# Kernel tuning notes

Measured on AMD Instinct MI355X. Metric: run time of the kernel, lower is better.

## Reference

```python
import jax, jax.numpy as jnp
import numpy as np

EPS = 1e-5

def _bin_act(x):
    # sign() forward, clipped straight-through estimator backward
    xc = jnp.clip(x, -1.0, 1.0)
    return xc + jax.lax.stop_gradient(jnp.sign(x) - xc)

def _bin_w(w):
    # XNOR-style: sign(w) scaled by per-output-channel mean(|w|); identity STE
    alpha = jnp.mean(jnp.abs(w), axis=(1, 2, 3), keepdims=True)
    return w + jax.lax.stop_gradient(jnp.sign(w) * alpha - w)

def _conv(x, w, stride, padding, groups):
    return jax.lax.conv_general_dilated(
        x, w, window_strides=(stride, stride),
        padding=[(padding, padding), (padding, padding)],
        feature_group_count=groups,
        dimension_numbers=('NCHW', 'OIHW', 'NCHW'))

def _binconv(x, w, stride, padding, groups):
    return _conv(_bin_act(x), _bin_w(w), stride, padding, groups)

def _bn(x, g, b, m, v):
    # eval-mode BatchNorm2d
    inv = g / jnp.sqrt(v + EPS)
    return x * inv[None, :, None, None] + (b - m * inv)[None, :, None, None]


def setup_inputs() -> dict:
    key = jax.random.key(0)
    ks = jax.random.split(key, 20)
    inp, oup = 256, 512
    d = {}
    d['x'] = jax.random.normal(ks[0], (64, inp, 28, 28), jnp.float32)
    d['w1'] = jax.random.normal(ks[1], (inp, 16, 3, 3), jnp.float32) * 0.1  # grouped, groups=inp/16
    d['w2'] = jax.random.normal(ks[2], (oup, inp, 1, 1), jnp.float32) * 0.05
    d['w3'] = jax.random.normal(ks[3], (oup, oup, 1, 1), jnp.float32) * 0.05
    for i, (name, c) in enumerate([('1', inp), ('2', oup), ('3', oup)]):
        d['g' + name] = jax.random.uniform(ks[4 + 4 * i], (c,), jnp.float32, 0.5, 1.5)
        d['b' + name] = jax.random.normal(ks[5 + 4 * i], (c,), jnp.float32) * 0.1
        d['m' + name] = jax.random.normal(ks[6 + 4 * i], (c,), jnp.float32) * 0.1
        d['v' + name] = jax.random.uniform(ks[7 + 4 * i], (c,), jnp.float32, 0.5, 1.5)
    return d


def reference(x, w1, w2, w3, g1, b1, m1, v1, g2, b2, m2, v2, g3, b3, m3, v3):
    inp = x.shape[1]
    groups = inp // 16
    # conv1 (binary grouped 3x3) + bn1 + residual + hardtanh
    out = _bn(_binconv(x, w1, 1, 1, groups), g1, b1, m1, v1)
    out = jnp.clip(out + x, -1.0, 1.0)
    # conv2 (binary 1x1, inp->oup) + bn2 + hardtanh
    out = jnp.clip(_bn(_binconv(out, w2, 1, 0, 1), g2, b2, m2, v2), -1.0, 1.0)
    res = out
    # conv3 (binary 1x1, oup->oup) + bn3 + residual + hardtanh
    out = _bn(_binconv(out, w3, 1, 0, 1), g3, b3, m3, v3)
    return jnp.clip(out + res, -1.0, 1.0)
```

## Files before the change

### kernel.cpp

```cpp
#include <hip/hip_runtime.h>
#include <stdint.h>

#define C1 256
#define C2 512
#define P_ 784
#define TAU 1e-6
#define PT 32
#define NT 25


__global__ __launch_bounds__(256) void prep(
    const float* __restrict__ w1, const float* __restrict__ w2, const float* __restrict__ w3,
    const float* __restrict__ g1, const float* __restrict__ b1, const float* __restrict__ m1, const float* __restrict__ v1,
    const float* __restrict__ g2, const float* __restrict__ b2, const float* __restrict__ m2, const float* __restrict__ v2,
    const float* __restrict__ g3, const float* __restrict__ b3, const float* __restrict__ m3, const float* __restrict__ v3,
    double* __restrict__ sc1d, double* __restrict__ bi1d,
    int* __restrict__ T2, float* __restrict__ sc2f, float* __restrict__ bi2f,
    float* __restrict__ sc3f, float* __restrict__ bi3f,
    uint16_t* __restrict__ wb1, uint32_t* __restrict__ bw2, uint32_t* __restrict__ bw3,
    unsigned long long* __restrict__ amin)
{
    int bid = blockIdx.x, t = threadIdx.x;
    if (bid == 0 && t == 0) amin[0] = ~0ULL;
    if (bid == 0) {
        int co = t;
        const float* wp = w1 + (size_t)co * 144;
        double s = 0.0;
        for (int k = 0; k < 144; k++) s += fabs((double)wp[k]);
        double alpha = s / 144.0;
        double iv = (double)g1[co] / sqrt((double)v1[co] + 1e-5);
        sc1d[co] = alpha * iv;
        bi1d[co] = (double)b1[co] - (double)m1[co] * iv;
        for (int tap = 0; tap < 9; tap++) {
            uint32_t wv = 0;
            for (int ci = 0; ci < 16; ci++) wv |= (uint32_t)(wp[ci * 9 + tap] < 0.f) << ci;
            wb1[co * 9 + tap] = (uint16_t)wv;
        }
    } else if (bid <= 2) {
        int co = (bid - 1) * 256 + t;
        const float* wp = w2 + (size_t)co * 256;
        double s = 0.0;
        for (int k = 0; k < 256; k++) s += fabs((double)wp[k]);
        double alpha = s / 256.0;
        double iv = (double)g2[co] / sqrt((double)v2[co] + 1e-5);
        double sc = alpha * iv;
        double bi = (double)b2[co] - (double)m2[co] * iv;
        int T = -257;
        while (T <= 257 && fma((double)T, sc, bi) < 0.0) T++;
        T2[co] = T;
        sc2f[co] = (float)sc;
        bi2f[co] = (float)bi;
        for (int wd = 0; wd < 8; wd++) {
            uint32_t wv = 0;
            for (int j = 0; j < 32; j++) wv |= (uint32_t)(wp[wd * 32 + j] < 0.f) << j;
            bw2[co * 8 + wd] = wv;
        }
    } else {
        int co = (bid - 3) * 256 + t;
        const float* wp = w3 + (size_t)co * 512;
        double s = 0.0;
        for (int k = 0; k < 512; k++) s += fabs((double)wp[k]);
        double alpha = s / 512.0;
        double iv = (double)g3[co] / sqrt((double)v3[co] + 1e-5);
        sc3f[co] = (float)(alpha * iv);
        bi3f[co] = (float)((double)b3[co] - (double)m3[co] * iv);
        for (int wd = 0; wd < 16; wd++) {
            uint32_t wv = 0;
            for (int j = 0; j < 32; j++) wv |= (uint32_t)(wp[wd * 32 + j] < 0.f) << j;
            bw3[co * 16 + wd] = wv;
        }
    }
}

__global__ __launch_bounds__(256) void k1(
    const float* __restrict__ x,
    const double* __restrict__ sc1d, const double* __restrict__ bi1d,
    const uint16_t* __restrict__ wb1,
    uint16_t* __restrict__ pk1, unsigned long long* __restrict__ amin)
{
    __shared__ uint32_t xzb[30][30];
    __shared__ uint16_t wbl[16][9];
    __shared__ double scs[16], bis[16];
    __shared__ float scf[16], bif[16];

    int g = blockIdx.x, n = blockIdx.y, t = threadIdx.x;

    for (int idx = t; idx < 900; idx += 256) ((uint32_t*)xzb)[idx] = 0;
    if (t < 144) ((uint16_t*)wbl)[t] = wb1[g * 144 + t];
    if (t < 16) {
        scs[t] = sc1d[g * 16 + t]; bis[t] = bi1d[g * 16 + t];
        scf[t] = (float)scs[t];    bif[t] = (float)bis[t];
    }
    __syncthreads();

    const float* xg = x + ((size_t)n * C1 + g * 16) * P_;
    float xr[4][16];
    #pragma unroll
    for (int i = 0; i < 4; i++) {
        int p = t + 256 * i;
        if (p < P_) {
            uint32_t sb = 0, nb = 0;
            #pragma unroll
            for (int ci = 0; ci < 16; ci++) {
                float xv = xg[ci * P_ + p];
                xr[i][ci] = xv;
                sb |= (uint32_t)(xv < 0.f) << ci;
                nb |= (uint32_t)(xv != 0.f) << ci;
            }
            int h = p / 28, w = p - 28 * h;
            xzb[h + 1][w + 1] = sb | (nb << 16);
        }
    }
    __syncthreads();

    uint16_t* pko = pk1 + ((size_t)n * 16 + g) * P_;
    #pragma unroll
    for (int i = 0; i < 4; i++) {
        int p = t + 256 * i;
        if (p < P_) {
            int h = p / 28, w = p - 28 * h;
            uint32_t xv9[9], zv9[9];
            int Z = 0;
            #pragma unroll
            for (int kh = 0; kh < 3; kh++)
                #pragma unroll
                for (int kw = 0; kw < 3; kw++) {
                    int k = kh * 3 + kw;
                    uint32_t xz = xzb[h + kh][w + kw];
                    xv9[k] = xz & 0xFFFFu;
                    zv9[k] = xz >> 16;
                    Z += __popc(zv9[k]);
                }
            uint32_t word = 0;
            #pragma unroll
            for (int co = 0; co < 16; co++) {
                int pd = 0;
                #pragma unroll
                for (int k = 0; k < 9; k++)
                    pd += __popc((xv9[k] ^ (uint32_t)wbl[co][k]) & zv9[k]);
                int S = Z - 2 * pd;
                float vf = __fmaf_rn((float)S, scf[co], bif[co]) + xr[i][co];
                uint32_t neg;
                if (fabsf(vf) < 1e-3f) {
                    double v = fma((double)S, scs[co], bis[co]) + (double)xr[i][co];
                    v = fmin(fmax(v, -1.0), 1.0);
                    double m = fabs(v);
                    if (m < TAU) {
                        unsigned long long pk =
                            ((unsigned long long)__float_as_uint((float)m) << 32) |
                            (unsigned long long)((uint32_t)(n * C1 + g * 16 + co) * (uint32_t)P_ + (uint32_t)p);
                        atomicMin(amin, pk);
                    }
                    neg = (v < 0.0);
                } else {
                    neg = (vf < 0.f);
                }
                word |= neg << co;
            }
            pko[p] = (uint16_t)word;
        }
    }
}

#define POP2(xp) (__popc((xp)[0] ^ wa.x) + __popc((xp)[1] ^ wa.y) + __popc((xp)[2] ^ wa.z) + __popc((xp)[3] ^ wa.w) \
                + __popc((xp)[4] ^ wb.x) + __popc((xp)[5] ^ wb.y) + __popc((xp)[6] ^ wb.z) + __popc((xp)[7] ^ wb.w))
#define POP3(yp) (__popc((yp)[0] ^ w3a.x) + __popc((yp)[1] ^ w3a.y) + __popc((yp)[2] ^ w3a.z) + __popc((yp)[3] ^ w3a.w) \
                + __popc((yp)[4] ^ w3b.x) + __popc((yp)[5] ^ w3b.y) + __popc((yp)[6] ^ w3b.z) + __popc((yp)[7] ^ w3b.w) \
                + __popc((yp)[8] ^ w3c.x) + __popc((yp)[9] ^ w3c.y) + __popc((yp)[10] ^ w3c.z) + __popc((yp)[11] ^ w3c.w) \
                + __popc((yp)[12] ^ w3d.x) + __popc((yp)[13] ^ w3d.y) + __popc((yp)[14] ^ w3d.z) + __popc((yp)[15] ^ w3d.w))

__global__ __launch_bounds__(512) void k23(
    const uint32_t* __restrict__ bw2, const uint32_t* __restrict__ bw3,
    const int* __restrict__ T2, const float* __restrict__ sc2f, const float* __restrict__ bi2f,
    const float* __restrict__ sc3f, const float* __restrict__ bi3f,
    const uint16_t* __restrict__ pk1, const unsigned long long* __restrict__ amin,
    float* __restrict__ out)
{
    __shared__ uint32_t xw2s[48 * 9];
    __shared__ uint32_t xw3s[48 * 17];
    uint16_t* raws = (uint16_t*)xw3s;

    int n = blockIdx.x, pc = blockIdx.y, t = threadIdx.x;
    int wv = t >> 6, lane = t & 63;
    bool wrap = (pc == NT - 1);
    int UN = wrap ? 32 : 48;

    const uint16_t* pkn = pk1 + (size_t)n * 16 * P_;
    for (int idx = t; idx < 16 * UN; idx += 512) {
        int g = idx / UN, i = idx - g * UN;
        int p = wrap ? (i < 16 ? 768 + i : i - 16) : 32 * pc + i;
        raws[g * 48 + i] = pkn[(size_t)g * P_ + p];
    }
    __syncthreads();
    if (t == 0) {
        unsigned long long a = amin[0];
        if (a != ~0ULL) {
            uint32_t loc = (uint32_t)a;
            uint32_t nn = loc / (C1 * P_);
            uint32_t rem = loc - nn * C1 * P_;
            uint32_t c = rem / P_;
            int p = (int)(rem - c * P_);
            if ((int)nn == n) {
                int i = -1;
                if (wrap) { if (p >= 768) i = p - 768; else if (p < 16) i = p + 16; }
                else { int d = p - 32 * pc; if (d >= 0 && d < 48) i = d; }
                if (i >= 0) raws[(c >> 4) * 48 + i] ^= (uint16_t)(1u << (c & 15));
            }
        }
    }
    __syncthreads();
    for (int idx = t; idx < UN * 8; idx += 512) {
        int i = idx >> 3, wd = idx & 7;
        xw2s[i * 9 + wd] = (uint32_t)raws[2 * wd * 48 + i] | ((uint32_t)raws[(2 * wd + 1) * 48 + i] << 16);
    }
    __syncthreads();

    int co = t;
    const uint4* w2q = (const uint4*)(bw2 + (size_t)co * 8);
    uint4 wa = w2q[0], wb = w2q[1];
    int Tv = T2[co];
    float sc2 = sc2f[co], bi2v = bi2f[co];
    const uint4* w3q = (const uint4*)(bw3 + (size_t)co * 16);
    uint4 w3a = w3q[0], w3b = w3q[1], w3c = w3q[2], w3d = w3q[3];
    float sc3 = sc3f[co], bi3v = bi3f[co];

    for (int i = 0; i < UN; i++) {
        const uint32_t* xp = xw2s + i * 9;
        int S = 256 - 2 * POP2(xp);
        unsigned long long mb = __ballot(S < Tv);
        if (lane == 0) {
            xw3s[i * 17 + 2 * wv]     = (uint32_t)mb;
            xw3s[i * 17 + 2 * wv + 1] = (uint32_t)(mb >> 32);
        }
    }
    __syncthreads();

    int par = co & 1;
    int pbase = wrap ? (par ? 0 : 768) : 32 * pc + 16 * par;
    int cnt = wrap ? 16 : 32;
    int i0 = par ? 16 : 0;
    float* op = out + ((size_t)n * C2 + co) * P_ + pbase;
    float4 b4;
    #pragma unroll 4
    for (int j = 0; j < cnt; j++) {
        int i = i0 + j;
        const uint32_t* xp = xw2s + i * 9;
        int S2 = 256 - 2 * POP2(xp);
        float r2 = fminf(fmaxf(__fmaf_rn((float)S2, sc2, bi2v), -1.f), 1.f);
        const uint32_t* yp = xw3s + i * 17;
        int S3 = 512 - 2 * POP3(yp);
        float v = __fmaf_rn((float)S3, sc3, bi3v) + r2;
        v = fminf(fmaxf(v, -1.f), 1.f);
        int r = j & 3;
        if (r == 0) b4.x = v; else if (r == 1) b4.y = v; else if (r == 2) b4.z = v;
        else { b4.w = v; ((float4*)op)[j >> 2] = b4; }
    }
}

extern "C" void kernel_launch(void* const* d_in, const int* in_sizes, int n_in,
                              void* d_out, int out_size, void* d_ws, size_t ws_size,
                              hipStream_t stream) {
    const float* x  = (const float*)d_in[0];
    const float* w1 = (const float*)d_in[1];
    const float* w2 = (const float*)d_in[2];
    const float* w3 = (const float*)d_in[3];
    const float* g1 = (const float*)d_in[4];
    const float* b1 = (const float*)d_in[5];
    const float* m1 = (const float*)d_in[6];
    const float* v1 = (const float*)d_in[7];
    const float* g2 = (const float*)d_in[8];
    const float* b2 = (const float*)d_in[9];
    const float* m2 = (const float*)d_in[10];
    const float* v2 = (const float*)d_in[11];
    const float* g3 = (const float*)d_in[12];
    const float* b3 = (const float*)d_in[13];
    const float* m3 = (const float*)d_in[14];
    const float* v3 = (const float*)d_in[15];
    float* out = (float*)d_out;

    char* ws = (char*)d_ws;
    unsigned long long* amin = (unsigned long long*)(ws + 0);
    double*   sc1d = (double*)(ws + 64);
    double*   bi1d = (double*)(ws + 2112);
    int*      T2   = (int*)(ws + 4160);
    float*    sc2f = (float*)(ws + 6208);
    float*    bi2f = (float*)(ws + 8256);
    float*    sc3f = (float*)(ws + 10304);
    float*    bi3f = (float*)(ws + 12352);
    uint16_t* wb1  = (uint16_t*)(ws + 14400);
    uint32_t* bw2  = (uint32_t*)(ws + 19008);
    uint32_t* bw3  = (uint32_t*)(ws + 35392);
    uint16_t* pk1  = (uint16_t*)(ws + 68160);

    prep<<<dim3(5), 256, 0, stream>>>(w1, w2, w3,
        g1, b1, m1, v1, g2, b2, m2, v2, g3, b3, m3, v3,
        sc1d, bi1d, T2, sc2f, bi2f, sc3f, bi3f, wb1, bw2, bw3, amin);
    k1<<<dim3(16, 64), 256, 0, stream>>>(x, sc1d, bi1d, wb1, pk1, amin);
    k23<<<dim3(64, NT), 512, 0, stream>>>(bw2, bw3, T2, sc2f, bi2f, sc3f, bi3f, pk1, amin, out);
}
```

Before: 153.4 us.

## Split fused conv2/conv3 kernel into separate passes via global bit-packed intermediate

Replaces the fused k23 kernel with two kernels. k2 computes the binarized conv2 output bits and writes them to a workspace buffer. k3 then tiles by 64 output channels over half-images and recomputes the conv2 residual before applying conv3. Each output channel now writes contiguous rows with float4 stores, and conv2 no longer has to be recomputed under the old overlapping 48/32 tiling. The cost is an extra launch and an extra global round trip for the intermediate. A fallback fused kernel with 56-pixel tiles runs when the workspace is too small.

Result: slower. 158.0 us (+3.0%).

```diff
diff --git a/kernel.cpp b/kernel.cpp
--- a/kernel.cpp
+++ b/kernel.cpp
@@ -5,9 +5,9 @@
 #define C2 512
 #define P_ 784
 #define TAU 1e-6
-#define PT 32
-#define NT 25
-
+#define HB 392
+
+#define WS_NEED 4885056
 
 __global__ __launch_bounds__(256) void prep(
     const float* __restrict__ w1, const float* __restrict__ w2, const float* __restrict__ w3,
@@ -169,27 +169,151 @@
                 + __popc((yp)[8] ^ w3c.x) + __popc((yp)[9] ^ w3c.y) + __popc((yp)[10] ^ w3c.z) + __popc((yp)[11] ^ w3c.w) \
                 + __popc((yp)[12] ^ w3d.x) + __popc((yp)[13] ^ w3d.y) + __popc((yp)[14] ^ w3d.z) + __popc((yp)[15] ^ w3d.w))
 
-__global__ __launch_bounds__(512) void k23(
+__global__ __launch_bounds__(512) void k2(
+    const uint32_t* __restrict__ bw2, const int* __restrict__ T2,
+    const uint16_t* __restrict__ pk1, const unsigned long long* __restrict__ amin,
+    uint32_t* __restrict__ xw3g)
+{
+    __shared__ uint16_t raws[16][56];
+    __shared__ uint32_t xw2s[56][8];
+    int pc = blockIdx.x, n = blockIdx.y, t = threadIdx.x;
+    int p0 = pc * 56, wv = t >> 6, lane = t & 63;
+
+    const uint32_t* pkw = (const uint32_t*)(pk1 + (size_t)n * 16 * P_);
+    for (int idx = t; idx < 16 * 28; idx += 512) {
+        int g = idx / 28, j = idx % 28;
+        ((uint32_t*)raws)[g * 28 + j] = pkw[g * (P_ / 2) + p0 / 2 + j];
+    }
+    __syncthreads();
+    if (t == 0) {
+        unsigned long long a = amin[0];
+        if (a != ~0ULL) {
+            uint32_t loc = (uint32_t)a;
+            uint32_t nn = loc / (C1 * P_);
+            uint32_t rem = loc - nn * C1 * P_;
+            uint32_t c = rem / P_, p = rem - c * P_;
+            if ((int)nn == n && (int)p >= p0 && (int)p < p0 + 56)
+                raws[c >> 4][p - p0] ^= (uint16_t)(1u << (c & 15));
+        }
+    }
+    __syncthreads();
+    for (int idx = t; idx < 56 * 8; idx += 512) {
+        int p = idx >> 3, wd = idx & 7;
+        xw2s[p][wd] = (uint32_t)raws[2 * wd][p] | ((uint32_t)raws[2 * wd + 1][p] << 16);
+    }
+    __syncthreads();
+
+    int co = t;
+    const uint4* w2q = (const uint4*)(bw2 + (size_t)co * 8);
+    uint4 wa = w2q[0], wb = w2q[1];
+    int Tv = T2[co];
+    uint32_t* xo = xw3g + ((size_t)n * P_ + p0) * 16;
+    #pragma unroll 4
+    for (int p = 0; p < 56; p++) {
+        const uint32_t* xp = xw2s[p];
+        int S = 256 - 2 * POP2(xp);
+        unsigned long long mb = __ballot(S < Tv);
+        if (lane == 0) {
+            xo[p * 16 + 2 * wv]     = (uint32_t)mb;
+            xo[p * 16 + 2 * wv + 1] = (uint32_t)(mb >> 32);
+        }
+    }
+}
+
+__global__ __launch_bounds__(512) void k3(
+    const uint32_t* __restrict__ bw2, const uint32_t* __restrict__ bw3,
+    const float* __restrict__ sc2f, const float* __restrict__ bi2f,
+    const float* __restrict__ sc3f, const float* __restrict__ bi3f,
+    const uint16_t* __restrict__ pk1, const uint32_t* __restrict__ xw3g,
+    const unsigned long long* __restrict__ amin,
+    float* __restrict__ out)
+{
+    __shared__ uint32_t xw2s[HB][9];
+    __shared__ uint32_t xw3s[HB][17];
+
+    int n = blockIdx.x, cc = blockIdx.y, t = threadIdx.x;
+    int co = cc * 64 + (t >> 3);
+    int sl = t & 7;
+
+    const uint4* w2q = (const uint4*)(bw2 + (size_t)co * 8);
+    uint4 wa = w2q[0], wb = w2q[1];
+    float sc2 = sc2f[co], bi2v = bi2f[co];
+    const uint4* w3q = (const uint4*)(bw3 + (size_t)co * 16);
+    uint4 w3a = w3q[0], w3b = w3q[1], w3c = w3q[2], w3d = w3q[3];
+    float sc3 = sc3f[co], bi3v = bi3f[co];
+
+    const uint16_t* pkn = pk1 + (size_t)n * 16 * P_;
+    const uint32_t* xg = xw3g + (size_t)n * P_ * 16;
+    float* op = out + ((size_t)n * C2 + co) * P_;
+
+    unsigned long long a = amin[0];
+
+    for (int half = 0; half < 2; half++) {
+        int pb = half * HB;
+        __syncthreads();
+        for (int idx = t; idx < HB * 8; idx += 512) {
+            int i = idx >> 3, wd = idx & 7;
+            int p = pb + i;
+            xw2s[i][wd] = (uint32_t)pkn[(size_t)(2 * wd) * P_ + p]
+                        | ((uint32_t)pkn[(size_t)(2 * wd + 1) * P_ + p] << 16);
+        }
+        for (int idx = t; idx < HB * 16; idx += 512) {
+            int i = idx >> 4, wd = idx & 15;
+            xw3s[i][wd] = xg[(size_t)(pb + i) * 16 + wd];
+        }
+        __syncthreads();
+        if (t == 0 && a != ~0ULL) {
+            uint32_t loc = (uint32_t)a;
+            uint32_t nn = loc / (C1 * P_);
+            uint32_t rem = loc - nn * C1 * P_;
+            uint32_t c = rem / P_;
+            int p = (int)(rem - c * P_);
+            if ((int)nn == n && p >= pb && p < pb + HB)
+                xw2s[p - pb][c >> 5] ^= 1u << (c & 31);
+        }
+        __syncthreads();
+
+        #pragma unroll 2
+        for (int j = 0; j < 13; j++) {
+            int i = sl * 4 + 32 * j;
+            if (i < HB) {
+                float4 b4;
+                #pragma unroll
+                for (int q = 0; q < 4; q++) {
+                    const uint32_t* xp = xw2s[i + q];
+                    int S2 = 256 - 2 * POP2(xp);
+                    float r2 = fminf(fmaxf(__fmaf_rn((float)S2, sc2, bi2v), -1.f), 1.f);
+                    const uint32_t* yp = xw3s[i + q];
+                    int S3 = 512 - 2 * POP3(yp);
+                    float v = __fmaf_rn((float)S3, sc3, bi3v) + r2;
+                    v = fminf(fmaxf(v, -1.f), 1.f);
+                    if (q == 0) b4.x = v; else if (q == 1) b4.y = v;
+                    else if (q == 2) b4.z = v; else b4.w = v;
+                }
+                *(float4*)(op + pb + i) = b4;
+            }
+        }
+    }
+}
+
+__global__ __launch_bounds__(512) void k23_fb(
     const uint32_t* __restrict__ bw2, const uint32_t* __restrict__ bw3,
     const int* __restrict__ T2, const float* __restrict__ sc2f, const float* __restrict__ bi2f,
     const float* __restrict__ sc3f, const float* __restrict__ bi3f,
     const uint16_t* __restrict__ pk1, const unsigned long long* __restrict__ amin,
     float* __restrict__ out)
 {
-    __shared__ uint32_t xw2s[48 * 9];
-    __shared__ uint32_t xw3s[48 * 17];
-    uint16_t* raws = (uint16_t*)xw3s;
-
-    int n = blockIdx.x, pc = blockIdx.y, t = threadIdx.x;
-    int wv = t >> 6, lane = t & 63;
-    bool wrap = (pc == NT - 1);
-    int UN = wrap ? 32 : 48;
-
-    const uint16_t* pkn = pk1 + (size_t)n * 16 * P_;
-    for (int idx = t; idx < 16 * UN; idx += 512) {
-        int g = idx / UN, i = idx - g * UN;
-        int p = wrap ? (i < 16 ? 768 + i : i - 16) : 32 * pc + i;
-        raws[g * 48 + i] = pkn[(size_t)g * P_ + p];
+    __shared__ uint16_t raws[16][56];
+    __shared__ uint32_t xw2[56][8];
+    __shared__ uint32_t xw3[56][16];
+
+    int pc = blockIdx.x, n = blockIdx.y, t = threadIdx.x;
+    int p0 = pc * 56, wv = t >> 6, lane = t & 63;
+
+    const uint32_t* pkw = (const uint32_t*)(pk1 + (size_t)n * 16 * P_);
+    for (int idx = t; idx < 16 * 28; idx += 512) {
+        int g = idx / 28, j = idx % 28;
+        ((uint32_t*)raws)[g * 28 + j] = pkw[g * (P_ / 2) + p0 / 2 + j];
     }
     __syncthreads();
     if (t == 0) {
@@ -198,62 +322,58 @@
             uint32_t loc = (uint32_t)a;
             uint32_t nn = loc / (C1 * P_);
             uint32_t rem = loc - nn * C1 * P_;
-            uint32_t c = rem / P_;
-            int p = (int)(rem - c * P_);
-            if ((int)nn == n) {
-                int i = -1;
-                if (wrap) { if (p >= 768) i = p - 768; else if (p < 16) i = p + 16; }
-                else { int d = p - 32 * pc; if (d >= 0 && d < 48) i = d; }
-                if (i >= 0) raws[(c >> 4) * 48 + i] ^= (uint16_t)(1u << (c & 15));
-            }
-        }
-    }
-    __syncthreads();
-    for (int idx = t; idx < UN * 8; idx += 512) {
-        int i = idx >> 3, wd = idx & 7;
-        xw2s[i * 9 + wd] = (uint32_t)raws[2 * wd * 48 + i] | ((uint32_t)raws[(2 * wd + 1) * 48 + i] << 16);
+            uint32_t c = rem / P_, p = rem - c * P_;
+            if ((int)nn == n && (int)p >= p0 && (int)p < p0 + 56)
+                raws[c >> 4][p - p0] ^= (uint16_t)(1u << (c & 15));
+        }
+    }
+    __syncthreads();
+    for (int idx = t; idx < 56 * 8; idx += 512) {
+        int p = idx >> 3, wd = idx & 7;
+        xw2[p][wd] = (uint32_t)raws[2 * wd][p] | ((uint32_t)raws[2 * wd + 1][p] << 16);
     }
     __syncthreads();
 
     int co = t;
-    const uint4* w2q = (const uint4*)(bw2 + (size_t)co * 8);
-    uint4 wa = w2q[0], wb = w2q[1];
+    uint4 wa, wb;
+    {
+        const uint4* w2q = (const uint4*)(bw2 + (size_t)co * 8);
+        wa = w2q[0]; wb = w2q[1];
+    }
     int Tv = T2[co];
     float sc2 = sc2f[co], bi2v = bi2f[co];
-    const uint4* w3q = (const uint4*)(bw3 + (size_t)co * 16);
-    uint4 w3a = w3q[0], w3b = w3q[1], w3c = w3q[2], w3d = w3q[3];
-    float sc3 = sc3f[co], bi3v = bi3f[co];
-
-    for (int i = 0; i < UN; i++) {
-        const uint32_t* xp = xw2s + i * 9;
+    float r2f[56];
+    #pragma unroll 4
+    for (int p = 0; p < 56; p++) {
+        const uint32_t* xp = xw2[p];
         int S = 256 - 2 * POP2(xp);
+        float vf = __fmaf_rn((float)S, sc2, bi2v);
+        r2f[p] = fminf(fmaxf(vf, -1.f), 1.f);
         unsigned long long mb = __ballot(S < Tv);
         if (lane == 0) {
-            xw3s[i * 17 + 2 * wv]     = (uint32_t)mb;
-            xw3s[i * 17 + 2 * wv + 1] = (uint32_t)(mb >> 32);
-        }
-    }
-    __syncthreads();
-
-    int par = co & 1;
-    int pbase = wrap ? (par ? 0 : 768) : 32 * pc + 16 * par;
-    int cnt = wrap ? 16 : 32;
-    int i0 = par ? 16 : 0;
-    float* op = out + ((size_t)n * C2 + co) * P_ + pbase;
+            xw3[p][2 * wv]     = (uint32_t)mb;
+            xw3[p][2 * wv + 1] = (uint32_t)(mb >> 32);
+        }
+    }
+    __syncthreads();
+
+    uint4 w3a, w3b, w3c, w3d;
+    {
+        const uint4* w3q = (const uint4*)(bw3 + (size_t)co * 16);
+        w3a = w3q[0]; w3b = w3q[1]; w3c = w3q[2]; w3d = w3q[3];
+    }
+    float sc3 = sc3f[co], bi3v = bi3f[co];
+    float* op = out + ((size_t)n * C2 + co) * P_ + p0;
     float4 b4;
     #pragma unroll 4
-    for (int j = 0; j < cnt; j++) {
-        int i = i0 + j;
-        const uint32_t* xp = xw2s + i * 9;
-        int S2 = 256 - 2 * POP2(xp);
-        float r2 = fminf(fmaxf(__fmaf_rn((float)S2, sc2, bi2v), -1.f), 1.f);
-        const uint32_t* yp = xw3s + i * 17;
+    for (int p = 0; p < 56; p++) {
+        const uint32_t* yp = xw3[p];
         int S3 = 512 - 2 * POP3(yp);
-        float v = __fmaf_rn((float)S3, sc3, bi3v) + r2;
+        float v = __fmaf_rn((float)S3, sc3, bi3v) + r2f[p];
         v = fminf(fmaxf(v, -1.f), 1.f);
-        int r = j & 3;
+        int r = p & 3;
         if (r == 0) b4.x = v; else if (r == 1) b4.y = v; else if (r == 2) b4.z = v;
-        else { b4.w = v; ((float4*)op)[j >> 2] = b4; }
+        else { b4.w = v; ((float4*)op)[p >> 2] = b4; }
     }
 }
 
@@ -291,10 +411,19 @@
     uint32_t* bw2  = (uint32_t*)(ws + 19008);
     uint32_t* bw3  = (uint32_t*)(ws + 35392);
     uint16_t* pk1  = (uint16_t*)(ws + 68160);
+    uint32_t* xw3g = (uint32_t*)(ws + 1673792);
 
     prep<<<dim3(5), 256, 0, stream>>>(w1, w2, w3,
         g1, b1, m1, v1, g2, b2, m2, v2, g3, b3, m3, v3,
         sc1d, bi1d, T2, sc2f, bi2f, sc3f, bi3f, wb1, bw2, bw3, amin);
     k1<<<dim3(16, 64), 256, 0, stream>>>(x, sc1d, bi1d, wb1, pk1, amin);
-    k23<<<dim3(64, NT), 512, 0, stream>>>(bw2, bw3, T2, sc2f, bi2f, sc3f, bi3f, pk1, amin, out);
-}
+
+    if (ws_size >= (size_t)WS_NEED) {
+        k2<<<dim3(14, 64), 512, 0, stream>>>(bw2, T2, pk1, amin, xw3g);
+        k3<<<dim3(64, 8), 512, 0, stream>>>(bw2, bw3, sc2f, bi2f, sc3f, bi3f,
+                                            pk1, xw3g, amin, out);
+    } else {
+        k23_fb<<<dim3(14, 64), 512, 0, stream>>>(bw2, bw3, T2, sc2f, bi2f, sc3f, bi3f,
+                                                 pk1, amin, out);
+    }
+}
```
